# Kernel optimization log

Measured on AMD Instinct MI355X. Metric: run time of the kernel, lower is better.

The kernel has to match this reference:

```python
import jax, jax.numpy as jnp
import numpy as np

H, D = 4, 32  # num_heads, per-head out dim (out_feats=128)
N_AGENT, N_GT, N_UAV = 50000, 50000, 50000
E = 600000
IN = 64


def _gat(x_src, x_dst, src, dst, W_src, W_dst, al, ar, W_res, b, num_dst):
    """DGL-style bipartite GATConv with residual, bias and ReLU activation."""
    fs = (x_src @ W_src).reshape(-1, H, D)      # [Ns,H,D]
    fd = (x_dst @ W_dst).reshape(-1, H, D)      # [Nd,H,D]
    el = jnp.sum(fs * al, axis=-1)              # [Ns,H]
    er = jnp.sum(fd * ar, axis=-1)              # [Nd,H]
    e = jax.nn.leaky_relu(el[src] + er[dst], 0.2)          # [E,H]
    # segment softmax over incoming edges of each dst node
    emax = jax.ops.segment_max(e, dst, num_segments=num_dst)   # [Nd,H], -inf for deg-0
    ee = jnp.exp(e - emax[dst])
    denom = jax.ops.segment_sum(ee, dst, num_segments=num_dst)
    a = ee / denom[dst]                          # [E,H]
    msg = fs[src] * a[:, :, None]                # [E,H,D]
    rst = jax.ops.segment_sum(msg, dst, num_segments=num_dst)  # [Nd,H,D]; zeros for deg-0
    res = (x_dst @ W_res).reshape(-1, H, D)      # residual projection
    out = jax.nn.relu(rst + res + b.reshape(1, H, D))
    return out.reshape(num_dst, H * D)


def setup_inputs() -> dict:
    key = jax.random.key(0)
    ks = jax.random.split(key, 20)
    s = 0.1  # weight init scale
    return {
        'x_gt': jax.random.normal(ks[0], (N_GT, IN), jnp.float32),
        'x_uav': jax.random.normal(ks[1], (N_UAV, IN), jnp.float32),
        'x_agent': jax.random.normal(ks[2], (N_AGENT, IN), jnp.float32),
        'src_gt': jax.random.randint(ks[3], (E,), 0, N_GT, jnp.int32),
        'dst_gt': jax.random.randint(ks[4], (E,), 0, N_AGENT, jnp.int32),
        'src_uav': jax.random.randint(ks[5], (E,), 0, N_UAV, jnp.int32),
        'dst_uav': jax.random.randint(ks[6], (E,), 0, N_AGENT, jnp.int32),
        'W_src_gt': s * jax.random.normal(ks[7], (IN, H * D), jnp.float32),
        'W_dst_gt': s * jax.random.normal(ks[8], (IN, H * D), jnp.float32),
        'attn_l_gt': s * jax.random.normal(ks[9], (H, D), jnp.float32),
        'attn_r_gt': s * jax.random.normal(ks[10], (H, D), jnp.float32),
        'W_res_gt': s * jax.random.normal(ks[11], (IN, H * D), jnp.float32),
        'b_gt': jnp.zeros((H * D,), jnp.float32),
        'W_src_uav': s * jax.random.normal(ks[12], (IN, H * D), jnp.float32),
        'W_dst_uav': s * jax.random.normal(ks[13], (IN, H * D), jnp.float32),
        'attn_l_uav': s * jax.random.normal(ks[14], (H, D), jnp.float32),
        'attn_r_uav': s * jax.random.normal(ks[15], (H, D), jnp.float32),
        'W_res_uav': s * jax.random.normal(ks[16], (IN, H * D), jnp.float32),
        'b_uav': jnp.zeros((H * D,), jnp.float32),
        'W_f': s * jax.random.normal(ks[17], (2 * H * D, H * D), jnp.float32),
        'b_f': jnp.zeros((H * D,), jnp.float32),
    }


def reference(x_gt, x_uav, x_agent, src_gt, dst_gt, src_uav, dst_uav,
              W_src_gt, W_dst_gt, attn_l_gt, attn_r_gt, W_res_gt, b_gt,
              W_src_uav, W_dst_uav, attn_l_uav, attn_r_uav, W_res_uav, b_uav,
              W_f, b_f):
    h_gt = _gat(x_gt, x_agent, src_gt, dst_gt, W_src_gt, W_dst_gt,
                attn_l_gt, attn_r_gt, W_res_gt, b_gt, N_AGENT)
    h_uav = _gat(x_uav, x_agent, src_uav, dst_uav, W_src_uav, W_dst_uav,
                 attn_l_uav, attn_r_uav, W_res_uav, b_uav, N_AGENT)
    h = jnp.concatenate([h_gt, h_uav], axis=1)   # [N_agent, 256]
    return jax.nn.relu(h @ W_f + b_f)            # [N_agent, 128]
```

## Files before the change

kernel.cpp:

```cpp
#include <hip/hip_runtime.h>
#include <hip/hip_bf16.h>

using bf16 = __hip_bfloat16;

#define NA 50000
#define NE 600000

typedef __attribute__((ext_vector_type(8))) short short8;
typedef __attribute__((ext_vector_type(4))) float f32x4;

#define HBUF_B   0u
#define FS_B     25600000u
#define EL_B     51200000u
#define RECS_B   54400000u
#define CNT_B    73600000u
#define ROW_B    74000000u
#define TOPS_B   74400016u
#define FLAG_B   74400528u
#define WST_GT_B 74400544u
#define WST_UAV_B 74416928u
#define WRT_B    74433312u
#define WFT_B    74466080u
#define ELT_GT_B 74531616u
#define ELT_UAV_B 74533664u
#define ERT_B    74535712u
#define RANK_B   74537760u
#define WS_BYTES 79337760u

__device__ __forceinline__ float b2f(bf16 v) { return __bfloat162float(v); }

__device__ __forceinline__ float ldf(const void* p, size_t i, int f32) {
    return f32 ? ((const float*)p)[i] : b2f(((const bf16*)p)[i]);
}

__device__ __forceinline__ unsigned short f2bs(float v) {
    bf16 t = __float2bfloat16(v);
    return *(unsigned short*)&t;
}

__device__ __forceinline__ float lrelu_exp(float v) {
    v = v > 0.f ? v : 0.2f * v;
    return __expf(v);
}

__device__ __forceinline__ unsigned int pack_bf16x2(float a, float b) {
    return (unsigned int)f2bs(a) | ((unsigned int)f2bs(b) << 16);
}

__device__ __forceinline__ float lo_f(unsigned int u) { return __uint_as_float(u << 16); }
__device__ __forceinline__ float hi_f(unsigned int u) { return __uint_as_float(u & 0xffff0000u); }

__device__ __forceinline__ short8 ldfrag8(const void* p, size_t off, int f32) {
    if (!f32) return *(const short8*)((const unsigned short*)p + off);
    union { short8 s; unsigned int u[4]; } r;
    const float* fp = (const float*)p + off;
#pragma unroll
    for (int j = 0; j < 4; ++j) r.u[j] = pack_bf16x2(fp[2 * j], fp[2 * j + 1]);
    return r.s;
}

__device__ int probe_f32(const void* x0) {
    __shared__ int cnt;
    if (threadIdx.x == 0) cnt = 0;
    __syncthreads();
    const bf16* p = (const bf16*)x0;
    int bad = 0;
    for (int i = threadIdx.x; i < 1024; i += 256) {
        float av = fabsf(b2f(p[i]));
        if (!(av <= 1e6f)) bad++;
    }
    if (bad) atomicAdd(&cnt, bad);
    __syncthreads();
    return cnt > 8;
}

__global__ void HeteroVisionConv_29703993819529_kernel(
    const void* x0,
    const void* Wsg, const void* alg, const void* Wdg, const void* arg_,
    const void* Wsu, const void* alu, const void* Wdu, const void* aru,
    const void* Wrg, const void* Wru, const void* Wf,
    unsigned short* wsT_gt, unsigned short* wsT_uav, unsigned short* wrT,
    unsigned short* wfT, unsigned short* elT_gt, unsigned short* elT_uav,
    unsigned short* erT,
    int* flag, unsigned int* outp, long sent) {
    int b = blockIdx.x, t = threadIdx.x;
    int f32 = probe_f32(x0);
    if (b == 20) {
        if (t == 0) { flag[0] = f32; outp[sent] = 0x447A447Au; }
        return;
    }
    if (b < 8) {
        for (int i = t; i < 16 * 256; i += 256) {
            int n = b * 16 + (i >> 8), k = i & 255;
            wfT[n * 256 + k] = f2bs(ldf(Wf, (size_t)k * 128 + n, f32));
        }
    } else if (b < 12) {
        for (int i = t; i < 64 * 64; i += 256) {
            int n = (b - 8) * 64 + (i >> 6), k = i & 63;
            float v = (n < 128) ? ldf(Wrg, (size_t)k * 128 + n, f32)
                                : ldf(Wru, (size_t)k * 128 + (n - 128), f32);
            wrT[n * 64 + k] = f2bs(v);
        }
    } else if (b < 14) {
        for (int i = t; i < 64 * 64; i += 256) {
            int n = (b - 12) * 64 + (i >> 6), k = i & 63;
            wsT_gt[n * 64 + k] = f2bs(ldf(Wsg, (size_t)k * 128 + n, f32));
        }
    } else if (b < 16) {
        for (int i = t; i < 64 * 64; i += 256) {
            int n = (b - 14) * 64 + (i >> 6), k = i & 63;
            wsT_uav[n * 64 + k] = f2bs(ldf(Wsu, (size_t)k * 128 + n, f32));
        }
    } else {
        int m = b - 16;
        const void* Wm = (m == 0) ? Wsg : (m == 1) ? Wdg : (m == 2) ? Wsu : Wdu;
        const void* Am = (m == 0) ? alg : (m == 1) ? arg_ : (m == 2) ? alu : aru;
        int k = t >> 2, h = t & 3;
        float a = 0.f;
        for (int d = 0; d < 32; ++d)
            a += ldf(Wm, (size_t)k * 128 + h * 32 + d, f32) *
                 ldf(Am, (size_t)h * 32 + d, f32);
        unsigned short v = f2bs(a);
        if (m == 0) {
            elT_gt[h * 64 + k] = v;
            for (int i = t; i < 12 * 64; i += 256) elT_gt[(4 + (i >> 6)) * 64 + (i & 63)] = 0;
        } else if (m == 2) {
            elT_uav[h * 64 + k] = v;
            for (int i = t; i < 12 * 64; i += 256) elT_uav[(4 + (i >> 6)) * 64 + (i & 63)] = 0;
        } else if (m == 1) {
            erT[h * 64 + k] = v;
        } else {
            erT[(4 + h) * 64 + k] = v;
            for (int i = t; i < 8 * 64; i += 256) erT[(8 + (i >> 6)) * 64 + (i & 63)] = 0;
        }
    }
}

__global__ void fused_k(const int* dg, const int* du,
                        unsigned int* cnt, unsigned int* rank,
                        const void* xg, const void* xu, const void* xa,
                        const unsigned short* wsT_gt, const unsigned short* wsT_uav,
                        const unsigned short* elT_gt, const unsigned short* elT_uav,
                        const unsigned short* wrT, const unsigned short* erT,
                        const void* bg, const void* bu,
                        float* elbase, bf16* fs, bf16* hbuf, const int* flag) {
    __shared__ unsigned short Bt[256 * 72];
    __shared__ float bl[256];
    int b = blockIdx.x, t = threadIdx.x;

    if (b < 3516 && (b % 3) == 0) {
        int idx = (b / 3) * 256 + t;
        if (idx >= 300000) return;
        int g = idx >= 150000;
        int e = (idx - g * 150000) * 4;
        int4 d4 = *(const int4*)((g ? du : dg) + e);
        unsigned int* c = cnt + g * NA;
        uint4 r4;
        r4.x = atomicAdd(&c[d4.x], 1u);
        r4.y = atomicAdd(&c[d4.y], 1u);
        r4.z = atomicAdd(&c[d4.z], 1u);
        r4.w = atomicAdd(&c[d4.w], 1u);
        *(uint4*)(rank + (size_t)g * NE + e) = r4;
        return;
    }
    int nidx = (b < 3516) ? (b - b / 3 - 1) : (2344 + (b - 3516));
    int f32 = *flag;
    int lane = t & 63, w = t >> 6;
    int m = lane & 15, quad = lane >> 4;

    if (nidx < 1564) {
        int g = nidx / 782, bb = nidx % 782;
        const void* A = g ? xu : xg;
        const unsigned short* WT = g ? wsT_uav : wsT_gt;
        const unsigned short* ET = g ? elT_uav : elT_gt;
        float* elout = elbase + (g ? 400000 : 0);
        bf16* out = fs + (size_t)g * NA * 128;
        for (int i = t * 8; i < 128 * 64; i += 256 * 8) {
            short8 v = *(const short8*)(WT + i);
            int n = i >> 6, k = i & 63;
            *(short8*)&Bt[n * 72 + k] = v;
        }
        __syncthreads();
        int row = bb * 64 + w * 16 + m;
        int rowc = row < NA ? row : NA - 1;
        short8 a0 = ldfrag8(A, (size_t)rowc * 64 + quad * 8, f32);
        short8 a1 = ldfrag8(A, (size_t)rowc * 64 + 32 + quad * 8, f32);
        f32x4 acc[8];
#pragma unroll
        for (int nt = 0; nt < 8; ++nt) acc[nt] = (f32x4){0.f, 0.f, 0.f, 0.f};
#pragma unroll
        for (int nt = 0; nt < 8; ++nt) {
            short8 b0 = *(const short8*)&Bt[(nt * 16 + m) * 72 + quad * 8];
            short8 b1 = *(const short8*)&Bt[(nt * 16 + m) * 72 + 32 + quad * 8];
            acc[nt] = __builtin_amdgcn_mfma_f32_16x16x32_bf16(a0, b0, acc[nt], 0, 0, 0);
            acc[nt] = __builtin_amdgcn_mfma_f32_16x16x32_bf16(a1, b1, acc[nt], 0, 0, 0);
        }
        f32x4 eacc = (f32x4){0.f, 0.f, 0.f, 0.f};
        {
            short8 e0 = *(const short8*)&ET[m * 64 + quad * 8];
            short8 e1 = *(const short8*)&ET[m * 64 + 32 + quad * 8];
            eacc = __builtin_amdgcn_mfma_f32_16x16x32_bf16(a0, e0, eacc, 0, 0, 0);
            eacc = __builtin_amdgcn_mfma_f32_16x16x32_bf16(a1, e1, eacc, 0, 0, 0);
        }
        int srow = bb * 64 + w * 16 + quad * 4;
#pragma unroll
        for (int nt = 0; nt < 8; ++nt) {
#pragma unroll
            for (int r = 0; r < 4; ++r) {
                int rr = srow + r;
                if (rr < NA) out[(size_t)rr * 128 + nt * 16 + m] = __float2bfloat16(acc[nt][r]);
            }
        }
        if (m < 4) {
#pragma unroll
            for (int r = 0; r < 4; ++r) {
                int rr = srow + r;
                if (rr < NA) elout[(size_t)rr * 4 + m] = eacc[r];
            }
        }
        return;
    }
    int bb = nidx - 1564;
    for (int i = t * 8; i < 256 * 64; i += 256 * 8) {
        short8 v = *(const short8*)(wrT + i);
        int n = i >> 6, k = i & 63;
        *(short8*)&Bt[n * 72 + k] = v;
    }
    bl[t] = (t < 128) ? ldf(bg, t, f32) : ldf(bu, t - 128, f32);
    __syncthreads();
    int row = bb * 64 + w * 16 + m;
    int rowc = row < NA ? row : NA - 1;
    short8 a0 = ldfrag8(xa, (size_t)rowc * 64 + quad * 8, f32);
    short8 a1 = ldfrag8(xa, (size_t)rowc * 64 + 32 + quad * 8, f32);
    f32x4 acc[16];
#pragma unroll
    for (int nt = 0; nt < 16; ++nt) acc[nt] = (f32x4){0.f, 0.f, 0.f, 0.f};
#pragma unroll
    for (int nt = 0; nt < 16; ++nt) {
        short8 b0 = *(const short8*)&Bt[(nt * 16 + m) * 72 + quad * 8];
        short8 b1 = *(const short8*)&Bt[(nt * 16 + m) * 72 + 32 + quad * 8];
        acc[nt] = __builtin_amdgcn_mfma_f32_16x16x32_bf16(a0, b0, acc[nt], 0, 0, 0);
        acc[nt] = __builtin_amdgcn_mfma_f32_16x16x32_bf16(a1, b1, acc[nt], 0, 0, 0);
    }
    f32x4 eacc = (f32x4){0.f, 0.f, 0.f, 0.f};
    {
        short8 e0 = *(const short8*)&erT[m * 64 + quad * 8];
        short8 e1 = *(const short8*)&erT[m * 64 + 32 + quad * 8];
        eacc = __builtin_amdgcn_mfma_f32_16x16x32_bf16(a0, e0, eacc, 0, 0, 0);
        eacc = __builtin_amdgcn_mfma_f32_16x16x32_bf16(a1, e1, eacc, 0, 0, 0);
    }
    int srow = bb * 64 + w * 16 + quad * 4;
#pragma unroll
    for (int nt = 0; nt < 16; ++nt) {
        int col = nt * 16 + m;
#pragma unroll
        for (int r = 0; r < 4; ++r) {
            int rr = srow + r;
            if (rr < NA)
                hbuf[(size_t)rr * 256 + col] = __float2bfloat16(acc[nt][r] + bl[col]);
        }
    }
    if (m < 8) {
        float* ero = (m < 4) ? (elbase + 200000) : (elbase + 600000);
        int mm = m & 3;
#pragma unroll
        for (int r = 0; r < 4; ++r) {
            int rr = srow + r;
            if (rr < NA) ero[(size_t)rr * 4 + mm] = eacc[r];
        }
    }
}

__global__ void scan1_k(const unsigned int* cnt, unsigned int* row, unsigned int* tops) {
    __shared__ unsigned int sh[256];
    int b = blockIdx.x, t = threadIdx.x;
    int base = b * 1024 + t * 4;
    unsigned int v[4];
    for (int j = 0; j < 4; ++j) v[j] = (base + j < 100000) ? cnt[base + j] : 0u;
    unsigned int s = v[0] + v[1] + v[2] + v[3];
    sh[t] = s;
    __syncthreads();
    for (int off = 1; off < 256; off <<= 1) {
        unsigned int x = (t >= off) ? sh[t - off] : 0u;
        __syncthreads();
        sh[t] += x;
        __syncthreads();
    }
    unsigned int run = sh[t] - s;
    for (int j = 0; j < 4; ++j) {
        if (base + j < 100000) row[base + j] = run;
        run += v[j];
    }
    if (t == 255) tops[b] = sh[255];
}

__global__ void scan2_k(unsigned int* tops, unsigned int* row) {
    __shared__ unsigned int sh[128];
    int t = threadIdx.x;
    unsigned int v = (t < 98) ? tops[t] : 0u;
    sh[t] = v;
    __syncthreads();
    for (int off = 1; off < 128; off <<= 1) {
        unsigned int x = (t >= off) ? sh[t - off] : 0u;
        __syncthreads();
        sh[t] += x;
        __syncthreads();
    }
    if (t < 98) tops[t] = sh[t] - v;
    if (t == 97) row[100000] = sh[97];
}

__global__ void scan3_k(unsigned int* row, const unsigned int* tops) {
    int b = blockIdx.x, t = threadIdx.x;
    unsigned int off = tops[b];
    for (int i = b * 1024 + t; i < b * 1024 + 1024; i += 256) {
        if (i < 100000) row[i] += off;
    }
}

__global__ void scatter_k(const int* sg, const int* dg, const int* su, const int* du,
                          const float* elbase, const unsigned int* row,
                          const unsigned int* rank, uint4* recs) {
    int idx = blockIdx.x * 256 + threadIdx.x;
    if (idx >= 2 * NE) return;
    int g = idx >= NE;
    int e = idx - g * NE;
    int s = (g ? su : sg)[e];
    int d = (g ? du : dg)[e];
    const float4* el4 = (const float4*)(elbase + (g ? 400000 : 0));
    const float4* er4 = (const float4*)(elbase + (g ? 600000 : 200000));
    unsigned int pos = row[g * NA + d] + rank[idx];
    float4 l = el4[s], r = er4[d];
    uint4 rec;
    rec.x = (unsigned int)s;
    rec.y = pack_bf16x2(lrelu_exp(l.x + r.x), lrelu_exp(l.y + r.y));
    rec.z = pack_bf16x2(lrelu_exp(l.z + r.z), lrelu_exp(l.w + r.w));
    rec.w = 0u;
    recs[pos] = rec;
}

__global__ void gather_k(const unsigned int* row, const uint4* recs,
                         const bf16* fs, bf16* hbuf) {
    int wid = (blockIdx.x * 256 + threadIdx.x) >> 6;
    int lane = threadIdx.x & 63;
    if (wid >= 2 * NA) return;
    int g = wid / NA, d = wid - g * NA;
    int eg = lane >> 4;
    int cl = lane & 15;
    int hsel = cl >> 3;
    int hodd = (cl >> 2) & 1;
    unsigned int start = row[g * NA + d];
    unsigned int end   = row[g * NA + d + 1];
    const uint4* fs4 = (const uint4*)(fs + (size_t)g * NA * 128);

    float denom = 0.f;
    float a[8];
#pragma unroll
    for (int k = 0; k < 8; ++k) a[k] = 0.f;

    if (start < end) {
        uint4 rr[4], rn[4];
#pragma unroll
        for (int j = 0; j < 4; ++j) {
            unsigned int idx = start + 4 * j + eg;
            rr[j] = recs[idx < end ? idx : end - 1];
        }
        for (unsigned int i = start; i < end; i += 16) {
            uint4 uu[4];
#pragma unroll
            for (int j = 0; j < 4; ++j) uu[j] = fs4[(size_t)rr[j].x * 16 + cl];
            unsigned int inext = i + 16;
#pragma unroll
            for (int j = 0; j < 4; ++j) {
                unsigned int idx = inext + 4 * j + eg;
                rn[j] = recs[idx < end ? idx : end - 1];
            }
#pragma unroll
            for (int j = 0; j < 4; ++j) {
                unsigned int idx = i + 4 * j + eg;
                unsigned int pp = hsel ? rr[j].z : rr[j].y;
                float e = hodd ? hi_f(pp) : lo_f(pp);
                if (idx >= end) e = 0.f;
                denom += e;
                a[0] += lo_f(uu[j].x) * e;
                a[1] += hi_f(uu[j].x) * e;
                a[2] += lo_f(uu[j].y) * e;
                a[3] += hi_f(uu[j].y) * e;
                a[4] += lo_f(uu[j].z) * e;
                a[5] += hi_f(uu[j].z) * e;
                a[6] += lo_f(uu[j].w) * e;
                a[7] += hi_f(uu[j].w) * e;
            }
#pragma unroll
            for (int j = 0; j < 4; ++j) rr[j] = rn[j];
        }
    }
#pragma unroll
    for (int k = 0; k < 8; ++k) {
        a[k] += __shfl_xor(a[k], 16, 64);
        a[k] += __shfl_xor(a[k], 32, 64);
    }
    denom += __shfl_xor(denom, 16, 64);
    denom += __shfl_xor(denom, 32, 64);
    if (lane < 16) {
        float inv = (end > start) ? 1.f / denom : 0.f;
        uint4* hp = (uint4*)(hbuf + (size_t)d * 256 + g * 128) + cl;
        uint4 rv = *hp;
        float v0 = a[0] * inv + lo_f(rv.x);
        float v1 = a[1] * inv + hi_f(rv.x);
        float v2 = a[2] * inv + lo_f(rv.y);
        float v3 = a[3] * inv + hi_f(rv.y);
        float v4 = a[4] * inv + lo_f(rv.z);
        float v5 = a[5] * inv + hi_f(rv.z);
        float v6 = a[6] * inv + lo_f(rv.w);
        float v7 = a[7] * inv + hi_f(rv.w);
        v0 = v0 > 0.f ? v0 : 0.f;
        v1 = v1 > 0.f ? v1 : 0.f;
        v2 = v2 > 0.f ? v2 : 0.f;
        v3 = v3 > 0.f ? v3 : 0.f;
        v4 = v4 > 0.f ? v4 : 0.f;
        v5 = v5 > 0.f ? v5 : 0.f;
        v6 = v6 > 0.f ? v6 : 0.f;
        v7 = v7 > 0.f ? v7 : 0.f;
        uint4 o;
        o.x = pack_bf16x2(v0, v1);
        o.y = pack_bf16x2(v2, v3);
        o.z = pack_bf16x2(v4, v5);
        o.w = pack_bf16x2(v6, v7);
        *hp = o;
    }
}

__global__ void final_k(const bf16* hbuf, const unsigned short* wfT,
                        const void* bfp, void* outp, const int* flag) {
    int f32 = *flag;
    int b = blockIdx.x;
    __shared__ unsigned short Bt[128 * 72];
    __shared__ float bl[128];
    int t = threadIdx.x;
    if (t < 128) bl[t] = ldf(bfp, t, f32);
    int lane = t & 63, w = t >> 6;
    int m = lane & 15, quad = lane >> 4;
    int row = b * 64 + w * 16 + m;
    int rowc = row < NA ? row : NA - 1;
    f32x4 acc[8];
#pragma unroll
    for (int nt = 0; nt < 8; ++nt) acc[nt] = (f32x4){0.f, 0.f, 0.f, 0.f};
    for (int kc = 0; kc < 4; ++kc) {
        __syncthreads();
        for (int i = t * 8; i < 128 * 64; i += 256 * 8) {
            int n = i >> 6, k = i & 63;
            short8 v = *(const short8*)(wfT + (size_t)n * 256 + kc * 64 + k);
            *(short8*)&Bt[n * 72 + k] = v;
        }
        __syncthreads();
        short8 a0 = *(const short8*)((const unsigned short*)hbuf +
                                     (size_t)rowc * 256 + kc * 64 + quad * 8);
        short8 a1 = *(const short8*)((const unsigned short*)hbuf +
                                     (size_t)rowc * 256 + kc * 64 + 32 + quad * 8);
#pragma unroll
        for (int nt = 0; nt < 8; ++nt) {
            short8 b0 = *(const short8*)&Bt[(nt * 16 + m) * 72 + quad * 8];
            short8 b1 = *(const short8*)&Bt[(nt * 16 + m) * 72 + 32 + quad * 8];
            acc[nt] = __builtin_amdgcn_mfma_f32_16x16x32_bf16(a0, b0, acc[nt], 0, 0, 0);
            acc[nt] = __builtin_amdgcn_mfma_f32_16x16x32_bf16(a1, b1, acc[nt], 0, 0, 0);
        }
    }
    int srow = b * 64 + w * 16 + quad * 4;
#pragma unroll
    for (int nt = 0; nt < 8; ++nt) {
        int col = nt * 16 + m;
        float bv = bl[col];
#pragma unroll
        for (int r = 0; r < 4; ++r) {
            int rr = srow + r;
            if (rr < NA) {
                float v = acc[nt][r] + bv;
                v = v > 0.f ? v : 0.f;
                if (f32) ((float*)outp)[(size_t)rr * 128 + col] = v;
                else ((bf16*)outp)[(size_t)rr * 128 + col] = __float2bfloat16(v);
            }
        }
    }
}

extern "C" void kernel_launch(void* const* d_in, const int* in_sizes, int n_in,
                              void* d_out, int out_size, void* d_ws, size_t ws_size,
                              hipStream_t stream) {
    const void* x_gt     = d_in[0];
    const void* x_uav    = d_in[1];
    const void* x_ag     = d_in[2];
    const int*  src_gt   = (const int*)d_in[3];
    const int*  dst_gt   = (const int*)d_in[4];
    const int*  src_uav  = (const int*)d_in[5];
    const int*  dst_uav  = (const int*)d_in[6];
    const void* Wsrc_gt  = d_in[7];
    const void* Wdst_gt  = d_in[8];
    const void* al_gt    = d_in[9];
    const void* ar_gt    = d_in[10];
    const void* Wres_gt  = d_in[11];
    const void* b_gt     = d_in[12];
    const void* Wsrc_uav = d_in[13];
    const void* Wdst_uav = d_in[14];
    const void* al_uav   = d_in[15];
    const void* ar_uav   = d_in[16];
    const void* Wres_uav = d_in[17];
    const void* b_uav    = d_in[18];
    const void* W_f      = d_in[19];
    const void* b_f      = d_in[20];

    char* wsb = (char*)d_ws;
    bf16* hbuf = (bf16*)(wsb + HBUF_B);
    bf16* fs = (bf16*)(wsb + FS_B);
    float* el = (float*)(wsb + EL_B);
    uint4* recs = (uint4*)(wsb + RECS_B);
    unsigned int* cnt = (unsigned int*)(wsb + CNT_B);
    unsigned int* row = (unsigned int*)(wsb + ROW_B);
    unsigned int* tops = (unsigned int*)(wsb + TOPS_B);
    int* flag = (int*)(wsb + FLAG_B);
    unsigned short* wsT_gt = (unsigned short*)(wsb + WST_GT_B);
    unsigned short* wsT_uav = (unsigned short*)(wsb + WST_UAV_B);
    unsigned short* wrT = (unsigned short*)(wsb + WRT_B);
    unsigned short* wfT = (unsigned short*)(wsb + WFT_B);
    unsigned short* elT_gt = (unsigned short*)(wsb + ELT_GT_B);
    unsigned short* elT_uav = (unsigned short*)(wsb + ELT_UAV_B);
    unsigned short* erT = (unsigned short*)(wsb + ERT_B);
    unsigned int* rank = (unsigned int*)(wsb + RANK_B);

    if (ws_size < (size_t)WS_BYTES) {
        hipMemsetAsync(d_out, 0x42, (size_t)out_size * 2, stream);
        return;
    }

    long sent = (long)out_size / 2 - 1;

    hipMemsetAsync(cnt, 0, 100000 * 4, stream);
    HeteroVisionConv_29703993819529_kernel<<<21, 256, 0, stream>>>(
        x_gt, Wsrc_gt, al_gt, Wdst_gt, ar_gt, Wsrc_uav, al_uav, Wdst_uav, ar_uav,
        Wres_gt, Wres_uav, W_f,
        wsT_gt, wsT_uav, wrT, wfT, elT_gt, elT_uav, erT,
        flag, (unsigned int*)d_out, sent);
    fused_k<<<3518, 256, 0, stream>>>(dst_gt, dst_uav, cnt, rank,
                                      x_gt, x_uav, x_ag,
                                      wsT_gt, wsT_uav, elT_gt, elT_uav,
                                      wrT, erT, b_gt, b_uav,
                                      el, fs, hbuf, flag);
    scan1_k<<<98, 256, 0, stream>>>(cnt, row, tops);
    scan2_k<<<1, 128, 0, stream>>>(tops, row);
    scan3_k<<<98, 256, 0, stream>>>(row, tops);
    scatter_k<<<4688, 256, 0, stream>>>(src_gt, dst_gt, src_uav, dst_uav,
                                        el, row, rank, recs);
    gather_k<<<25000, 256, 0, stream>>>(row, recs, fs, hbuf);
    final_k<<<782, 256, 0, stream>>>(hbuf, wfT, b_f, d_out, flag);
}
```

Baseline: 298.0 us.

## Privatize degree counters per XCC and shrink edge records to 12 bytes

The degree-counting atomics now go into a separate counter array for each XCC, selected by reading the hardware XCC id. They use workgroup scope, so they no longer contend across the die as device-scope atomics would. scan1 folds the eight per-XCC counts into exclusive offsets, and scatter adds the XCC offset decoded from a tag stored in the rank. Edge records also shrink from uint4 to uint3, which cuts scatter and gather traffic. The risks are that workgroup-scope atomics from several CUs on the same XCC may not be coherent through L2 in every case, and the 12-byte records lose 16-byte alignment.

```diff
diff --git a/kernel.cpp b/kernel.cpp
--- a/kernel.cpp
+++ b/kernel.cpp
@@ -13,19 +13,19 @@
 #define FS_B     25600000u
 #define EL_B     51200000u
 #define RECS_B   54400000u
-#define CNT_B    73600000u
-#define ROW_B    74000000u
-#define TOPS_B   74400016u
-#define FLAG_B   74400528u
-#define WST_GT_B 74400544u
-#define WST_UAV_B 74416928u
-#define WRT_B    74433312u
-#define WFT_B    74466080u
-#define ELT_GT_B 74531616u
-#define ELT_UAV_B 74533664u
-#define ERT_B    74535712u
-#define RANK_B   74537760u
-#define WS_BYTES 79337760u
+#define CNT_B    68800000u
+#define ROW_B    72000000u
+#define TOPS_B   72400016u
+#define FLAG_B   72400528u
+#define WST_GT_B 72400544u
+#define WST_UAV_B 72416928u
+#define WRT_B    72433312u
+#define WFT_B    72466080u
+#define ELT_GT_B 72531616u
+#define ELT_UAV_B 72533664u
+#define ERT_B    72535712u
+#define RANK_B   72537760u
+#define WS_BYTES 77337760u
 
 __device__ __forceinline__ float b2f(bf16 v) { return __bfloat162float(v); }
 
@@ -57,6 +57,12 @@
 #pragma unroll
     for (int j = 0; j < 4; ++j) r.u[j] = pack_bf16x2(fp[2 * j], fp[2 * j + 1]);
     return r.s;
+}
+
+__device__ __forceinline__ unsigned int xcc_id() {
+    unsigned int x;
+    asm volatile("s_getreg_b32 %0, hwreg(HW_REG_XCC_ID)" : "=s"(x));
+    return x & 7u;
 }
 
 __device__ int probe_f32(const void* x0) {
@@ -154,12 +160,19 @@
         int g = idx >= 150000;
         int e = (idx - g * 150000) * 4;
         int4 d4 = *(const int4*)((g ? du : dg) + e);
-        unsigned int* c = cnt + g * NA;
+        unsigned int xcc = xcc_id();
+        unsigned int* c = cnt + xcc * 100000 + g * NA;
         uint4 r4;
-        r4.x = atomicAdd(&c[d4.x], 1u);
-        r4.y = atomicAdd(&c[d4.y], 1u);
-        r4.z = atomicAdd(&c[d4.z], 1u);
-        r4.w = atomicAdd(&c[d4.w], 1u);
+        r4.x = __hip_atomic_fetch_add(&c[d4.x], 1u, __ATOMIC_RELAXED,
+                                      __HIP_MEMORY_SCOPE_WORKGROUP);
+        r4.y = __hip_atomic_fetch_add(&c[d4.y], 1u, __ATOMIC_RELAXED,
+                                      __HIP_MEMORY_SCOPE_WORKGROUP);
+        r4.z = __hip_atomic_fetch_add(&c[d4.z], 1u, __ATOMIC_RELAXED,
+                                      __HIP_MEMORY_SCOPE_WORKGROUP);
+        r4.w = __hip_atomic_fetch_add(&c[d4.w], 1u, __ATOMIC_RELAXED,
+                                      __HIP_MEMORY_SCOPE_WORKGROUP);
+        unsigned int tag = xcc << 24;
+        r4.x |= tag; r4.y |= tag; r4.z |= tag; r4.w |= tag;
         *(uint4*)(rank + (size_t)g * NE + e) = r4;
         return;
     }
@@ -271,12 +284,24 @@
     }
 }
 
-__global__ void scan1_k(const unsigned int* cnt, unsigned int* row, unsigned int* tops) {
+__global__ void scan1_k(unsigned int* cnt, unsigned int* row, unsigned int* tops) {
     __shared__ unsigned int sh[256];
     int b = blockIdx.x, t = threadIdx.x;
     int base = b * 1024 + t * 4;
     unsigned int v[4];
-    for (int j = 0; j < 4; ++j) v[j] = (base + j < 100000) ? cnt[base + j] : 0u;
+    for (int j = 0; j < 4; ++j) {
+        int d = base + j;
+        unsigned int tot = 0u;
+        if (d < 100000) {
+#pragma unroll
+            for (int x = 0; x < 8; ++x) {
+                unsigned int c = cnt[x * 100000 + d];
+                cnt[x * 100000 + d] = tot;
+                tot += c;
+            }
+        }
+        v[j] = tot;
+    }
     unsigned int s = v[0] + v[1] + v[2] + v[3];
     sh[t] = s;
     __syncthreads();
@@ -320,7 +345,8 @@
 
 __global__ void scatter_k(const int* sg, const int* dg, const int* su, const int* du,
                           const float* elbase, const unsigned int* row,
-                          const unsigned int* rank, uint4* recs) {
+                          const unsigned int* cnt, const unsigned int* rank,
+                          unsigned int* recs) {
     int idx = blockIdx.x * 256 + threadIdx.x;
     if (idx >= 2 * NE) return;
     int g = idx >= NE;
@@ -329,17 +355,18 @@
     int d = (g ? du : dg)[e];
     const float4* el4 = (const float4*)(elbase + (g ? 400000 : 0));
     const float4* er4 = (const float4*)(elbase + (g ? 600000 : 200000));
-    unsigned int pos = row[g * NA + d] + rank[idx];
+    unsigned int rk = rank[idx];
+    unsigned int xcc = rk >> 24, lr = rk & 0xFFFFFFu;
+    unsigned int pos = row[g * NA + d] + cnt[xcc * 100000 + g * NA + d] + lr;
     float4 l = el4[s], r = er4[d];
-    uint4 rec;
+    uint3 rec;
     rec.x = (unsigned int)s;
     rec.y = pack_bf16x2(lrelu_exp(l.x + r.x), lrelu_exp(l.y + r.y));
     rec.z = pack_bf16x2(lrelu_exp(l.z + r.z), lrelu_exp(l.w + r.w));
-    rec.w = 0u;
-    recs[pos] = rec;
-}
-
-__global__ void gather_k(const unsigned int* row, const uint4* recs,
+    *(uint3*)(recs + (size_t)pos * 3) = rec;
+}
+
+__global__ void gather_k(const unsigned int* row, const unsigned int* recs,
                          const bf16* fs, bf16* hbuf) {
     int wid = (blockIdx.x * 256 + threadIdx.x) >> 6;
     int lane = threadIdx.x & 63;
@@ -359,11 +386,11 @@
     for (int k = 0; k < 8; ++k) a[k] = 0.f;
 
     if (start < end) {
-        uint4 rr[4], rn[4];
+        uint3 rr[4], rn[4];
 #pragma unroll
         for (int j = 0; j < 4; ++j) {
             unsigned int idx = start + 4 * j + eg;
-            rr[j] = recs[idx < end ? idx : end - 1];
+            rr[j] = *(const uint3*)(recs + (size_t)(idx < end ? idx : end - 1) * 3);
         }
         for (unsigned int i = start; i < end; i += 16) {
             uint4 uu[4];
@@ -373,7 +400,7 @@
 #pragma unroll
             for (int j = 0; j < 4; ++j) {
                 unsigned int idx = inext + 4 * j + eg;
-                rn[j] = recs[idx < end ? idx : end - 1];
+                rn[j] = *(const uint3*)(recs + (size_t)(idx < end ? idx : end - 1) * 3);
             }
 #pragma unroll
             for (int j = 0; j < 4; ++j) {
@@ -513,7 +540,7 @@
     bf16* hbuf = (bf16*)(wsb + HBUF_B);
     bf16* fs = (bf16*)(wsb + FS_B);
     float* el = (float*)(wsb + EL_B);
-    uint4* recs = (uint4*)(wsb + RECS_B);
+    unsigned int* recs = (unsigned int*)(wsb + RECS_B);
     unsigned int* cnt = (unsigned int*)(wsb + CNT_B);
     unsigned int* row = (unsigned int*)(wsb + ROW_B);
     unsigned int* tops = (unsigned int*)(wsb + TOPS_B);
@@ -534,7 +561,7 @@
 
     long sent = (long)out_size / 2 - 1;
 
-    hipMemsetAsync(cnt, 0, 100000 * 4, stream);
+    hipMemsetAsync(cnt, 0, 8 * 100000 * 4, stream);
     HeteroVisionConv_29703993819529_kernel<<<21, 256, 0, stream>>>(
         x_gt, Wsrc_gt, al_gt, Wdst_gt, ar_gt, Wsrc_uav, al_uav, Wdst_uav, ar_uav,
         Wres_gt, Wres_uav, W_f,
@@ -549,7 +576,7 @@
     scan2_k<<<1, 128, 0, stream>>>(tops, row);
     scan3_k<<<98, 256, 0, stream>>>(row, tops);
     scatter_k<<<4688, 256, 0, stream>>>(src_gt, dst_gt, src_uav, dst_uav,
-                                        el, row, rank, recs);
+                                        el, row, cnt, rank, recs);
     gather_k<<<25000, 256, 0, stream>>>(row, recs, fs, hbuf);
     final_k<<<782, 256, 0, stream>>>(hbuf, wfT, b_f, d_out, flag);
 }
```

Result: no change. 299.3 us (+0.4%).
